# Optimization experiments

Hardware: AMD Instinct MI355X
Metric: run time of the kernel (lower is better)

The kernel has to match this reference:

```python
import jax, jax.numpy as jnp
import numpy as np

NUM_GROUPS = 32
EPS = 1e-5
NUM_HEAD = 8
DIM_HEAD = 64


def group_norm(t, w, b):
    # t: (B, N, C) tokens; GroupNorm over (N, C//G) within each group
    B, N, C = t.shape
    g = t.reshape(B, N, NUM_GROUPS, C // NUM_GROUPS)
    mu = g.mean(axis=(1, 3), keepdims=True)
    var = g.var(axis=(1, 3), keepdims=True)
    g = (g - mu) * jax.lax.rsqrt(var + EPS)
    return g.reshape(B, N, C) * w + b


def setup_inputs() -> dict:
    key = jax.random.key(0)
    ks = jax.random.split(key, 4)
    B, C, H, W = 2, 512, 48, 48
    hidden = NUM_HEAD * DIM_HEAD
    return {
        "x": jax.random.normal(ks[0], (B, C, H, W), dtype=jnp.float32),
        "gn1_w": jnp.ones((C,), jnp.float32),
        "gn1_b": jnp.zeros((C,), jnp.float32),
        "w_qkv": jax.random.normal(ks[1], (3 * hidden, C), jnp.float32) * 0.02,
        "mem_kv": jax.random.normal(ks[2], (2, NUM_HEAD, DIM_HEAD, 4), jnp.float32),
        "w_out": jax.random.normal(ks[3], (C, hidden), jnp.float32) * 0.02,
        "b_out": jnp.zeros((C,), jnp.float32),
        "gn2_w": jnp.ones((C,), jnp.float32),
        "gn2_b": jnp.zeros((C,), jnp.float32),
    }


def reference(x, gn1_w, gn1_b, w_qkv, mem_kv, w_out, b_out, gn2_w, gn2_b):
    B, C, H, W = x.shape
    N = H * W
    hidden = NUM_HEAD * DIM_HEAD
    scale = DIM_HEAD ** -0.5

    # tokens: (B, N, C)
    t = x.reshape(B, C, N).transpose(0, 2, 1)
    t = group_norm(t, gn1_w, gn1_b)

    # 1x1 conv QKV projection == per-token GEMM
    qkv = t @ w_qkv.T  # (B, N, 3*hidden)
    q, k, v = jnp.split(qkv, 3, axis=-1)

    def to_heads(a):  # (B, N, hidden) -> (B, nh, N, dh)
        return a.reshape(B, N, NUM_HEAD, DIM_HEAD).transpose(0, 2, 1, 3)

    q, k, v = to_heads(q), to_heads(k), to_heads(v)

    # memory kv prepended along sequence axis: (nh, dh, nkv) -> (1, nh, nkv, dh)
    mk = jnp.broadcast_to(mem_kv[0].transpose(0, 2, 1)[None], (B, NUM_HEAD, mem_kv.shape[-1], DIM_HEAD))
    mv = jnp.broadcast_to(mem_kv[1].transpose(0, 2, 1)[None], (B, NUM_HEAD, mem_kv.shape[-1], DIM_HEAD))
    k = jnp.concatenate([mk, k], axis=2)
    v = jnp.concatenate([mv, v], axis=2)

    scores = jnp.einsum('bhid,bhjd->bhij', q, k) * scale  # (B, nh, N, N+nkv)
    attn = jax.nn.softmax(scores, axis=-1)  # dropout = identity in eval
    o = jnp.einsum('bhij,bhjd->bhid', attn, v)  # (B, nh, N, dh)

    o = o.transpose(0, 2, 1, 3).reshape(B, N, hidden)
    o = o @ w_out.T + b_out  # 1x1 out conv
    o = group_norm(o, gn2_w, gn2_b)
    return o.transpose(0, 2, 1).reshape(B, C, H, W)
```

## Files before the change

### kernel.cpp

```cpp
#include <hip/hip_runtime.h>
#include <hip/hip_bf16.h>

typedef short short8 __attribute__((ext_vector_type(8)));
typedef short short4b __attribute__((ext_vector_type(4)));
typedef float f32x4 __attribute__((ext_vector_type(4)));

#define GPTR(x) ((const __attribute__((address_space(1))) void*)(x))
#define LPTR(x) ((__attribute__((address_space(3))) void*)(x))

static __device__ __forceinline__ unsigned short f2bf(float f) {
  __hip_bfloat16 h = __float2bfloat16(f);
  return __builtin_bit_cast(unsigned short, h);
}
static __device__ __forceinline__ float bf2f(unsigned short u) {
  unsigned int v = ((unsigned int)u) << 16;
  return __builtin_bit_cast(float, v);
}
static __device__ __forceinline__ float fexp2(float x) {
#if __has_builtin(__builtin_amdgcn_exp2f)
  return __builtin_amdgcn_exp2f(x);
#else
  return exp2f(x);
#endif
}
static __device__ __forceinline__ short bftrunc(float f) {
  return (short)(__builtin_bit_cast(unsigned int, f) >> 16);
}

static __device__ __forceinline__ void block_reduce2(float& s, float& q) {
#pragma unroll
  for (int o = 32; o > 0; o >>= 1) { s += __shfl_down(s, o); q += __shfl_down(q, o); }
  __shared__ float rs[4], rq[4];
  int tid = threadIdx.x;
  if ((tid & 63) == 0) { rs[tid >> 6] = s; rq[tid >> 6] = q; }
  __syncthreads();
  if (tid == 0) {
    s = rs[0] + rs[1] + rs[2] + rs[3];
    q = rq[0] + rq[1] + rq[2] + rq[3];
  }
}

__global__ __launch_bounds__(256) void gn1_stats_kernel(const float* __restrict__ x,
                                                        float2* __restrict__ part1) {
  int bgc = blockIdx.x;
  const float4* base = (const float4*)x + (size_t)bgc * 1152;
  float s = 0.f, q = 0.f;
  for (int i = threadIdx.x; i < 1152; i += 256) {
    float4 v = base[i];
    s += v.x + v.y + v.z + v.w;
    q += v.x * v.x + v.y * v.y + v.z * v.z + v.w * v.w;
  }
  block_reduce2(s, q);
  if (threadIdx.x == 0) part1[bgc] = make_float2(s, q);
}

__global__ __launch_bounds__(256) void tnorm_prep_kernel(const float* __restrict__ x,
    const float* __restrict__ gw, const float* __restrict__ gb,
    const float2* __restrict__ part1, unsigned short* __restrict__ t,
    const float* __restrict__ wqkv, const float* __restrict__ wout,
    const float* __restrict__ memkv,
    unsigned short* __restrict__ wq, unsigned short* __restrict__ wo,
    unsigned short* __restrict__ Kb, unsigned short* __restrict__ Vt) {
  __shared__ float tile[32][33];
  int blk = blockIdx.x;
  if (blk < 2304) {
    int n0 = (blk % 72) * 32, c0 = ((blk / 72) & 15) * 32, b = blk / 1152;
    int g0 = c0 >> 4;
    float mu2[2], rs2[2];
#pragma unroll
    for (int gg = 0; gg < 2; gg++) {
      float s = 0.f, q = 0.f;
      const float2* p = part1 + (size_t)(b * 32 + g0 + gg) * 8;
#pragma unroll
      for (int k = 0; k < 8; k++) { float2 v = p[k]; s += v.x; q += v.y; }
      float mu = s / 36864.f;
      float var = q / 36864.f - mu * mu;
      mu2[gg] = mu;
      rs2[gg] = rsqrtf(var + 1e-5f);
    }
    int tx = threadIdx.x & 31, ty = threadIdx.x >> 5;
#pragma unroll
    for (int r = 0; r < 4; r++) {
      int c = c0 + ty + r * 8;
      tile[ty + r * 8][tx] = x[((size_t)(b * 512 + c)) * 2304 + n0 + tx];
    }
    __syncthreads();
    int gg = tx >> 4;
#pragma unroll
    for (int r = 0; r < 4; r++) {
      int n = n0 + ty + r * 8;
      int c = c0 + tx;
      float v = tile[tx][ty + r * 8];
      t[((size_t)(b * 2304 + n)) * 512 + c] = f2bf((v - mu2[gg]) * rs2[gg] * gw[c] + gb[c]);
    }
  } else {
    int i = (blk - 2304) * 256 + threadIdx.x;
    if (i < 786432) {
      wq[i] = f2bf(wqkv[i]);
    } else if (i < 1048576) {
      int j = i - 786432;
      wo[j] = f2bf(wout[j]);
    } else if (i < 1056768) {
      int tt = i - 1048576;
      int d = tt & 63, j = (tt >> 6) & 3, h = (tt >> 8) & 7, b = (tt >> 11) & 1, s = tt >> 12;
      unsigned short bv = f2bf(memkv[((s * 8 + h) * 64 + d) * 4 + j]);
      if (s == 0) Kb[((size_t)(b * 8 + h) * 2308 + j) * 64 + d] = bv;
      else        Vt[((size_t)(b * 8 + h) * 64 + d) * 2368 + j] = bv;
    }
  }
}

__global__ __launch_bounds__(256) void gemm_qkv_kernel(
    const unsigned short* __restrict__ A, const unsigned short* __restrict__ Bw,
    unsigned short* __restrict__ Qb, unsigned short* __restrict__ Kb,
    unsigned short* __restrict__ Vt) {
  __shared__ __attribute__((aligned(16))) unsigned short As[64 * 32];
  __shared__ __attribute__((aligned(16))) unsigned short Bs[128 * 32];
  int m0 = blockIdx.x * 64, o0 = blockIdx.y * 128;
  int tid = threadIdx.x, lane = tid & 63, wave = tid >> 6;
  int quad = lane >> 4, l15 = lane & 15;
  int wm = wave & 1, wn = wave >> 1;
  const float CS = 0.18033688011112042f;
  f32x4 acc[2][4] = {};
  for (int k0 = 0; k0 < 512; k0 += 32) {
    __syncthreads();
    {
      int row = tid >> 2, cc = tid & 3;
      __builtin_amdgcn_global_load_lds(GPTR(A + (size_t)(m0 + row) * 512 + k0 + cc * 8),
                                       LPTR(As + tid * 8), 16, 0, 0);
    }
#pragma unroll
    for (int c = 0; c < 2; c++) {
      int q = tid + c * 256;
      int row = q >> 2, cc = q & 3;
      __builtin_amdgcn_global_load_lds(GPTR(Bw + (size_t)(o0 + row) * 512 + k0 + cc * 8),
                                       LPTR(Bs + q * 8), 16, 0, 0);
    }
    __syncthreads();
    short8 af[2], bf[4];
#pragma unroll
    for (int i = 0; i < 2; i++) af[i] = *(const short8*)(As + (wm * 32 + i * 16 + l15) * 32 + quad * 8);
#pragma unroll
    for (int j = 0; j < 4; j++) bf[j] = *(const short8*)(Bs + (wn * 64 + j * 16 + l15) * 32 + quad * 8);
#pragma unroll
    for (int i = 0; i < 2; i++)
#pragma unroll
      for (int j = 0; j < 4; j++)
        acc[i][j] = __builtin_amdgcn_mfma_f32_16x16x32_bf16(af[i], bf[j], acc[i][j], 0, 0, 0);
  }
#pragma unroll
  for (int i = 0; i < 2; i++) {
#pragma unroll
    for (int j = 0; j < 4; j++) {
      int colo = o0 + wn * 64 + j * 16 + l15;
      int part = colo >> 9, rr = colo & 511, h = rr >> 6, d = rr & 63;
      int mbase = m0 + wm * 32 + i * 16 + quad * 4;
      int b = (mbase >= 2304) ? 1 : 0;
      int n = mbase - b * 2304;
      if (part == 0) {
#pragma unroll
        for (int reg = 0; reg < 4; reg++)
          Qb[((size_t)(b * 8 + h) * 2304 + n + reg) * 64 + d] = f2bf(acc[i][j][reg] * CS);
      } else if (part == 1) {
#pragma unroll
        for (int reg = 0; reg < 4; reg++)
          Kb[((size_t)(b * 8 + h) * 2308 + 4 + n + reg) * 64 + d] = f2bf(acc[i][j][reg]);
      } else {
        unsigned short bv[4];
#pragma unroll
        for (int reg = 0; reg < 4; reg++) bv[reg] = f2bf(acc[i][j][reg]);
        unsigned long long pk = (unsigned long long)bv[0] | ((unsigned long long)bv[1] << 16) |
                                ((unsigned long long)bv[2] << 32) | ((unsigned long long)bv[3] << 48);
        *(unsigned long long*)(Vt + ((size_t)(b * 8 + h) * 64 + d) * 2368 + 4 + n) = pk;
      }
    }
  }
}

__global__ __launch_bounds__(256) void attn_kernel(
    const unsigned short* __restrict__ Qb, const unsigned short* __restrict__ Kb,
    const unsigned short* __restrict__ Vt,
    unsigned short* __restrict__ Opart, float* __restrict__ Lbuf) {
  __shared__ __attribute__((aligned(16))) unsigned short Ks[64 * 72];
  __shared__ __attribute__((aligned(16))) unsigned short Vts[64 * 68];
  int qt = blockIdx.x, bh = blockIdx.y, sp = blockIdx.z;
  int m0 = qt * 64;
  int kt0 = sp * 10, kt1 = (kt0 + 10 < 37) ? kt0 + 10 : 37;
  const unsigned short* Qh = Qb + (size_t)bh * 2304 * 64;
  const unsigned short* Kh = Kb + (size_t)bh * 2308 * 64;
  const unsigned short* VtH = Vt + (size_t)bh * 64 * 2368;
  int tid = threadIdx.x, lane = tid & 63, wave = tid >> 6;
  int quad = lane >> 4, l15 = lane & 15;

  short8 qf[2];
#pragma unroll
  for (int s = 0; s < 2; s++)
    qf[s] = *(const short8*)(Qh + (size_t)(m0 + wave * 16 + l15) * 64 + s * 32 + quad * 8);

  f32x4 oacc[4] = {};
  float lsumT = 0.f;

  for (int kt = kt0; kt < kt1; kt++) {
    __syncthreads();
#pragma unroll
    for (int c = 0; c < 2; c++) {
      int q = tid + c * 256;
      int krow = q >> 3, c8 = q & 7;
      int gk = kt * 64 + krow;
      uint4 kv = make_uint4(0, 0, 0, 0);
      if (gk < 2308) kv = *(const uint4*)(Kh + (size_t)gk * 64 + c8 * 8);
      *(uint4*)(Ks + krow * 72 + c8 * 8) = kv;
      uint4 vv = *(const uint4*)(VtH + (size_t)krow * 2368 + kt * 64 + c8 * 8);
      *(uint4*)(Vts + krow * 68 + c8 * 8) = vv;
    }
    __syncthreads();
    short4b pt[4];
#pragma unroll
    for (int jn = 0; jn < 4; jn++) {
      f32x4 st = {};
#pragma unroll
      for (int s = 0; s < 2; s++) {
        short8 kf = *(const short8*)(Ks + (jn * 16 + l15) * 72 + s * 32 + quad * 8);
        st = __builtin_amdgcn_mfma_f32_16x16x32_bf16(kf, qf[s], st, 0, 0, 0);
      }
#pragma unroll
      for (int r = 0; r < 4; r++) {
        float p = fexp2(st[r]);
        if (kt == 36 && (jn * 16 + quad * 4 + r) >= 4) p = 0.f;
        lsumT += p;
        pt[jn][r] = bftrunc(p);
      }
    }
#pragma unroll
    for (int jn = 0; jn < 4; jn++) {
#pragma unroll
      for (int jo = 0; jo < 4; jo++) {
        short4b vf = *(const short4b*)(Vts + (jo * 16 + l15) * 68 + jn * 16 + quad * 4);
        oacc[jo] = __builtin_amdgcn_mfma_f32_16x16x16bf16_1k(pt[jn], vf, oacc[jo], 0, 0, 0);
      }
    }
  }
  size_t obase = (size_t)(sp * 16 + bh) * 2304;
  {
    float v = lsumT;
    v += __shfl_xor(v, 16);
    v += __shfl_xor(v, 32);
    if (quad == 0) Lbuf[obase + m0 + wave * 16 + l15] = v;
  }
#pragma unroll
  for (int r = 0; r < 4; r++) {
    int row = m0 + wave * 16 + quad * 4 + r;
#pragma unroll
    for (int jo = 0; jo < 4; jo++)
      Opart[(obase + row) * 64 + jo * 16 + l15] = f2bf(oacc[jo][r]);
  }
}

__global__ __launch_bounds__(256) void combine_kernel(
    const unsigned short* __restrict__ Opart, const float* __restrict__ Lbuf,
    unsigned short* __restrict__ Ot, float* __restrict__ p2s, float* __restrict__ p2q) {
  int t = threadIdx.x;
  if (blockIdx.x == 0 && t < 128) {
    if (t < 64) p2s[t] = 0.f;
    else        p2q[t - 64] = 0.f;
  }
  int rg = blockIdx.x * 16 + (t >> 4);
  int d4 = (t & 15) * 4;
  int bh = rg / 2304, row = rg - bh * 2304;
  int b = bh >> 3, h = bh & 7;
  float den = 0.f, num[4] = {};
#pragma unroll
  for (int s = 0; s < 4; s++) {
    size_t ri = ((size_t)(s * 16 + bh) * 2304 + row);
    den += Lbuf[ri];
    uint2 pv = *(const uint2*)(Opart + ri * 64 + d4);
    const unsigned short* pp = (const unsigned short*)&pv;
#pragma unroll
    for (int k = 0; k < 4; k++) num[k] += bf2f(pp[k]);
  }
  float rinv = 1.f / den;
  unsigned short ov[4];
#pragma unroll
  for (int k = 0; k < 4; k++) ov[k] = f2bf(num[k] * rinv);
  *(uint2*)(Ot + ((size_t)(b * 2304 + row)) * 512 + h * 64 + d4) = *(uint2*)ov;
}

__global__ __launch_bounds__(256) void gemm_out_kernel(
    const unsigned short* __restrict__ A, const unsigned short* __restrict__ Bw,
    const float* __restrict__ bias, float* __restrict__ y,
    float* __restrict__ p2s, float* __restrict__ p2q) {
  __shared__ __attribute__((aligned(16))) unsigned short As[64 * 32];
  __shared__ __attribute__((aligned(16))) unsigned short Bs[128 * 32];
  __shared__ float sgrp[8], qgrp[8];
  int m0 = blockIdx.x * 64, o0 = blockIdx.y * 128;
  int tid = threadIdx.x, lane = tid & 63, wave = tid >> 6;
  int quad = lane >> 4, l15 = lane & 15;
  int wm = wave & 1, wn = wave >> 1;
  if (tid < 8) { sgrp[tid] = 0.f; qgrp[tid] = 0.f; }
  f32x4 acc[2][4] = {};
  for (int k0 = 0; k0 < 512; k0 += 32) {
    __syncthreads();
    {
      int row = tid >> 2, cc = tid & 3;
      __builtin_amdgcn_global_load_lds(GPTR(A + (size_t)(m0 + row) * 512 + k0 + cc * 8),
                                       LPTR(As + tid * 8), 16, 0, 0);
    }
#pragma unroll
    for (int c = 0; c < 2; c++) {
      int q = tid + c * 256;
      int row = q >> 2, cc = q & 3;
      __builtin_amdgcn_global_load_lds(GPTR(Bw + (size_t)(o0 + row) * 512 + k0 + cc * 8),
                                       LPTR(Bs + q * 8), 16, 0, 0);
    }
    __syncthreads();
    short8 af[2], bf[4];
#pragma unroll
    for (int i = 0; i < 2; i++) af[i] = *(const short8*)(As + (wm * 32 + i * 16 + l15) * 32 + quad * 8);
#pragma unroll
    for (int j = 0; j < 4; j++) bf[j] = *(const short8*)(Bs + (wn * 64 + j * 16 + l15) * 32 + quad * 8);
#pragma unroll
    for (int i = 0; i < 2; i++)
#pragma unroll
      for (int j = 0; j < 4; j++)
        acc[i][j] = __builtin_amdgcn_mfma_f32_16x16x32_bf16(af[i], bf[j], acc[i][j], 0, 0, 0);
  }
  float ss[4] = {}, qq[4] = {};
#pragma unroll
  for (int i = 0; i < 2; i++) {
#pragma unroll
    for (int j = 0; j < 4; j++) {
      int colo = o0 + wn * 64 + j * 16 + l15;
      float bb = bias[colo];
#pragma unroll
      for (int reg = 0; reg < 4; reg++) {
        int m = m0 + wm * 32 + i * 16 + quad * 4 + reg;
        float v = acc[i][j][reg] + bb;
        y[(size_t)m * 512 + colo] = v;
        ss[j] += v;
        qq[j] += v * v;
      }
    }
  }
#pragma unroll
  for (int j = 0; j < 4; j++) {
#pragma unroll
    for (int o = 1; o < 64; o <<= 1) { ss[j] += __shfl_xor(ss[j], o); qq[j] += __shfl_xor(qq[j], o); }
  }
  if (lane == 0) {
#pragma unroll
    for (int j = 0; j < 4; j++) {
      atomicAdd(&sgrp[wn * 4 + j], ss[j]);
      atomicAdd(&qgrp[wn * 4 + j], qq[j]);
    }
  }
  __syncthreads();
  if (tid < 8) {
    int b = (m0 >= 2304) ? 1 : 0;
    int g = b * 32 + (o0 >> 4) + tid;
    atomicAdd(&p2s[g], sgrp[tid]);
    atomicAdd(&p2q[g], qgrp[tid]);
  }
}

__global__ __launch_bounds__(256) void gn2_final_kernel(const float* __restrict__ y,
    const float* __restrict__ gw, const float* __restrict__ gb,
    const float* __restrict__ p2s, const float* __restrict__ p2q,
    float* __restrict__ out) {
  __shared__ float tile[32][33];
  int n0 = blockIdx.x * 32, c0 = blockIdx.y * 32, b = blockIdx.z;
  int g0 = c0 >> 4;
  float mu2[2], rs2[2];
#pragma unroll
  for (int gg = 0; gg < 2; gg++) {
    float s = p2s[b * 32 + g0 + gg], q = p2q[b * 32 + g0 + gg];
    float mu = s / 36864.f;
    float var = q / 36864.f - mu * mu;
    mu2[gg] = mu;
    rs2[gg] = rsqrtf(var + 1e-5f);
  }
  int tx = threadIdx.x & 31, ty = threadIdx.x >> 5;
#pragma unroll
  for (int r = 0; r < 4; r++) {
    int n = n0 + ty + r * 8;
    tile[ty + r * 8][tx] = y[((size_t)(b * 2304 + n)) * 512 + c0 + tx];
  }
  __syncthreads();
#pragma unroll
  for (int r = 0; r < 4; r++) {
    int c = c0 + ty + r * 8;
    int gg = (ty + r * 8) >> 4;
    float v = tile[tx][ty + r * 8];
    out[((size_t)(b * 512 + c)) * 2304 + n0 + tx] = (v - mu2[gg]) * rs2[gg] * gw[c] + gb[c];
  }
}

extern "C" void kernel_launch(void* const* d_in, const int* in_sizes, int n_in,
                              void* d_out, int out_size, void* d_ws, size_t ws_size,
                              hipStream_t stream) {
  const float* x     = (const float*)d_in[0];
  const float* gn1w  = (const float*)d_in[1];
  const float* gn1b  = (const float*)d_in[2];
  const float* wqkv  = (const float*)d_in[3];
  const float* memkv = (const float*)d_in[4];
  const float* wout  = (const float*)d_in[5];
  const float* bout  = (const float*)d_in[6];
  const float* gn2w  = (const float*)d_in[7];
  const float* gn2b  = (const float*)d_in[8];
  float* out = (float*)d_out;

  char* ws = (char*)d_ws;
  float2* part1        = (float2*)(ws + 0);
  float* p2s           = (float*)(ws + 4096);
  float* p2q           = (float*)(ws + 4352);
  unsigned short* wqB  = (unsigned short*)(ws + 69632);
  unsigned short* woB  = (unsigned short*)(ws + 1642496);
  unsigned short* tB   = (unsigned short*)(ws + 2166784);
  unsigned short* Qb   = (unsigned short*)(ws + 6885376);
  unsigned short* Kb   = (unsigned short*)(ws + 11603968);
  unsigned short* Ot   = (unsigned short*)(ws + 21057536);
  float* y             = (float*)(ws + 25776128);
  unsigned short* Vt   = (unsigned short*)(ws + 35213312);
  unsigned short* Opart= (unsigned short*)(ws + 40062976);
  float* Lbuf          = (float*)(ws + 58937344);

  gn1_stats_kernel<<<512, 256, 0, stream>>>(x, part1);
  tnorm_prep_kernel<<<6432, 256, 0, stream>>>(x, gn1w, gn1b, part1, tB,
                                              wqkv, wout, memkv, wqB, woB, Kb, Vt);
  gemm_qkv_kernel<<<dim3(72, 12), 256, 0, stream>>>(tB, wqB, Qb, Kb, Vt);
  attn_kernel<<<dim3(36, 16, 4), 256, 0, stream>>>(Qb, Kb, Vt, Opart, Lbuf);
  combine_kernel<<<2304, 256, 0, stream>>>(Opart, Lbuf, Ot, p2s, p2q);
  gemm_out_kernel<<<dim3(72, 4), 256, 0, stream>>>(Ot, woB, bout, y, p2s, p2q);
  gn2_final_kernel<<<dim3(72, 16, 2), 256, 0, stream>>>(y, gn2w, gn2b, p2s, p2q, out);
}
```

Measured before the change: 161.5 us.

## Fuse split-K attention combine into attention kernel via last-block atomic counter

Removes the separate combine kernel launch. Each attention block now increments a per-(query tile, head) atomic counter after writing its partial output, and the last of the four splits reduces the partials into Ot. A memset zeroes the counters and the GN2 accumulators that the combine kernel used to clear. This saves one launch and lets the combine overlap with other attention blocks, at the cost of thread fences, atomics and an extra memset call.

```diff
diff --git a/kernel.cpp b/kernel.cpp
--- a/kernel.cpp
+++ b/kernel.cpp
@@ -180,7 +180,8 @@
 __global__ __launch_bounds__(256) void attn_kernel(
     const unsigned short* __restrict__ Qb, const unsigned short* __restrict__ Kb,
     const unsigned short* __restrict__ Vt,
-    unsigned short* __restrict__ Opart, float* __restrict__ Lbuf) {
+    unsigned short* __restrict__ Opart, float* __restrict__ Lbuf,
+    unsigned short* __restrict__ Ot, int* __restrict__ cnt) {
   __shared__ __attribute__((aligned(16))) unsigned short Ks[64 * 72];
   __shared__ __attribute__((aligned(16))) unsigned short Vts[64 * 68];
   int qt = blockIdx.x, bh = blockIdx.y, sp = blockIdx.z;
@@ -254,35 +255,34 @@
     for (int jo = 0; jo < 4; jo++)
       Opart[(obase + row) * 64 + jo * 16 + l15] = f2bf(oacc[jo][r]);
   }
-}
-
-__global__ __launch_bounds__(256) void combine_kernel(
-    const unsigned short* __restrict__ Opart, const float* __restrict__ Lbuf,
-    unsigned short* __restrict__ Ot, float* __restrict__ p2s, float* __restrict__ p2q) {
-  int t = threadIdx.x;
-  if (blockIdx.x == 0 && t < 128) {
-    if (t < 64) p2s[t] = 0.f;
-    else        p2q[t - 64] = 0.f;
-  }
-  int rg = blockIdx.x * 16 + (t >> 4);
-  int d4 = (t & 15) * 4;
-  int bh = rg / 2304, row = rg - bh * 2304;
-  int b = bh >> 3, h = bh & 7;
-  float den = 0.f, num[4] = {};
-#pragma unroll
-  for (int s = 0; s < 4; s++) {
-    size_t ri = ((size_t)(s * 16 + bh) * 2304 + row);
-    den += Lbuf[ri];
-    uint2 pv = *(const uint2*)(Opart + ri * 64 + d4);
-    const unsigned short* pp = (const unsigned short*)&pv;
-#pragma unroll
-    for (int k = 0; k < 4; k++) num[k] += bf2f(pp[k]);
-  }
-  float rinv = 1.f / den;
-  unsigned short ov[4];
-#pragma unroll
-  for (int k = 0; k < 4; k++) ov[k] = f2bf(num[k] * rinv);
-  *(uint2*)(Ot + ((size_t)(b * 2304 + row)) * 512 + h * 64 + d4) = *(uint2*)ov;
+  __threadfence();
+  __shared__ int lastFlag;
+  if (tid == 0) lastFlag = (atomicAdd(&cnt[qt * 16 + bh], 1) == 3);
+  __syncthreads();
+  if (lastFlag) {
+    __threadfence();
+    int b = bh >> 3, h = bh & 7;
+    int d4 = (tid & 15) * 4;
+#pragma unroll
+    for (int i = 0; i < 4; i++) {
+      int gr = m0 + (tid >> 4) + i * 16;
+      float den = 0.f, num[4] = {};
+#pragma unroll
+      for (int s = 0; s < 4; s++) {
+        size_t ri = ((size_t)(s * 16 + bh) * 2304 + gr);
+        den += Lbuf[ri];
+        uint2 pv = *(const uint2*)(Opart + ri * 64 + d4);
+        const unsigned short* pp = (const unsigned short*)&pv;
+#pragma unroll
+        for (int k = 0; k < 4; k++) num[k] += bf2f(pp[k]);
+      }
+      float rinv = 1.f / den;
+      unsigned short ov[4];
+#pragma unroll
+      for (int k = 0; k < 4; k++) ov[k] = f2bf(num[k] * rinv);
+      *(uint2*)(Ot + ((size_t)(b * 2304 + gr)) * 512 + h * 64 + d4) = *(uint2*)ov;
+    }
+  }
 }
 
 __global__ __launch_bounds__(256) void gemm_out_kernel(
@@ -412,6 +412,7 @@
   float2* part1        = (float2*)(ws + 0);
   float* p2s           = (float*)(ws + 4096);
   float* p2q           = (float*)(ws + 4352);
+  int* cnt             = (int*)(ws + 4608);
   unsigned short* wqB  = (unsigned short*)(ws + 69632);
   unsigned short* woB  = (unsigned short*)(ws + 1642496);
   unsigned short* tB   = (unsigned short*)(ws + 2166784);
@@ -423,12 +424,12 @@
   unsigned short* Opart= (unsigned short*)(ws + 40062976);
   float* Lbuf          = (float*)(ws + 58937344);
 
+  hipMemsetAsync(ws + 4096, 0, 2816, stream);
   gn1_stats_kernel<<<512, 256, 0, stream>>>(x, part1);
   tnorm_prep_kernel<<<6432, 256, 0, stream>>>(x, gn1w, gn1b, part1, tB,
                                               wqkv, wout, memkv, wqB, woB, Kb, Vt);
   gemm_qkv_kernel<<<dim3(72, 12), 256, 0, stream>>>(tB, wqB, Qb, Kb, Vt);
-  attn_kernel<<<dim3(36, 16, 4), 256, 0, stream>>>(Qb, Kb, Vt, Opart, Lbuf);
-  combine_kernel<<<2304, 256, 0, stream>>>(Opart, Lbuf, Ot, p2s, p2q);
+  attn_kernel<<<dim3(36, 16, 4), 256, 0, stream>>>(Qb, Kb, Vt, Opart, Lbuf, Ot, cnt);
   gemm_out_kernel<<<dim3(72, 4), 256, 0, stream>>>(Ot, woB, bout, y, p2s, p2q);
   gn2_final_kernel<<<dim3(72, 16, 2), 256, 0, stream>>>(y, gn2w, gn2b, p2s, p2q, out);
 }
```

After: 510.2 us. 216% more time.
